# Performance work log

Measured on AMD Instinct MI355X. Metric: run time of the kernel, lower is better.

The kernel has to match this reference:

```python
import jax, jax.numpy as jnp
import numpy as np

B, S, D = 32, 256, 128
K = 16          # num_sample (negatives + the positive appended last)
V = 50000       # vocab / num_classes


def setup_inputs() -> dict:
    key = jax.random.key(0)
    k1, k2, k3, k4 = jax.random.split(key, 4)
    return {
        "input_latent": jax.random.normal(k1, (B, S, D), dtype=jnp.float32),
        "target_labels": jax.random.randint(k2, (B, S), 0, V, dtype=jnp.int64),
        "batch_samples": jax.random.randint(k3, (B, S * (K - 1)), 0, V, dtype=jnp.int64),
        "embed_weight": jax.random.normal(k4, (V, D), dtype=jnp.float32),
    }


def reference(input_latent, target_labels, batch_samples, embed_weight):
    b, s, d = input_latent.shape
    out_emb = embed_weight[target_labels]                      # [B,S,D] positives
    neg_emb = embed_weight[batch_samples].reshape(b, s, K - 1, d)
    # Candidates per target position j: K-1 negatives + the positive itself (last)
    samples = jnp.concatenate([neg_emb, out_emb[:, :, None, :]], axis=2)  # [B,S,K,D]
    # sample_rep[b,i,j,k] = latent[b,i] . samples[b,j,k]
    sample_scores = jnp.einsum('bid,bjkd->bijk', input_latent, samples)   # [B,S,S,K]
    # output_rep[b,i,j] = latent[b,i] . out_emb[b,j] (== sample_scores[...,K-1])
    out_scores = jnp.einsum('bid,bjd->bij', input_latent, out_emb)        # [B,S,S]
    # log( exp(out - max) / sum_k exp(sample - max) ) = out - logsumexp(sample)
    lse = jax.scipy.special.logsumexp(sample_scores, axis=3)              # [B,S,S]
    return out_scores - lse
```

## Files before the change

kernel.cpp:

```cpp
#include <hip/hip_runtime.h>
#include <hip/hip_bf16.h>
#include <math.h>

#define BB 32
#define SS 256
#define DD 128
#define KK 16
#define VV 50000
#define SK (SS*KK)

typedef __attribute__((ext_vector_type(8))) short bf16x8;
typedef __attribute__((ext_vector_type(4))) float f32x4;
typedef __attribute__((ext_vector_type(16))) float f32x16;
typedef unsigned short ushort_t;

static __device__ __forceinline__ short f2bf(float f) {
    __hip_bfloat16 h = __float2bfloat16(f);
    return *(short*)&h;
}

static __device__ __forceinline__ int lds_off(int row, int d) {
    return row * 256 + ((d * 2) ^ ((row & 15) << 4));
}

static __device__ __forceinline__ void gload_lds16(const void* g, void* lds) {
    __builtin_amdgcn_global_load_lds(
        (const __attribute__((address_space(1))) unsigned int*)g,
        (__attribute__((address_space(3))) unsigned int*)lds, 16, 0, 0);
}

#define NLAT (BB*SS*DD)
#define NCHUNK_LAT (NLAT/8)

__global__ __launch_bounds__(256)
void convert_lat_kernel(const float* __restrict__ latent,
                        ushort_t* __restrict__ ws_lat)
{
    int i = blockIdx.x * 256 + threadIdx.x;
    if (i >= NCHUNK_LAT) return;
    const float* src = latent + (size_t)i * 8;
    float f[8];
    *(float4*)(f + 0) = ((const float4*)src)[0];
    *(float4*)(f + 4) = ((const float4*)src)[1];
    short o[8];
    #pragma unroll
    for (int e = 0; e < 8; ++e) o[e] = f2bf(f[e]);
    *(bf16x8*)(ws_lat + (size_t)i * 8) = *(bf16x8*)o;
}

#define MTB 128
#define NT  128

__global__ __launch_bounds__(256, 5)
void neg_loss_main(const ushort_t* __restrict__ lat_bf,
                   const int*      __restrict__ labels,
                   const int*      __restrict__ samples,
                   const float*    __restrict__ embed,
                   float* __restrict__ out)
{
    __shared__ char ldsA[MTB * 256];

    const int b    = blockIdx.z;
    const int m0   = blockIdx.y * MTB;
    const int n0   = blockIdx.x * NT;
    const int tid  = threadIdx.x;
    const int wave = tid >> 6;
    const int lane = tid & 63;
    const int q    = lane & 15;
    const int sub  = lane >> 4;
    const int l31  = lane & 31;
    const int hi   = lane >> 5;

    #pragma unroll
    for (int t = 0; t < 8; ++t) {
        const int r0 = wave * 32 + t * 4;
        const int r  = r0 + sub;
        const ushort_t* src = lat_bf + ((size_t)(b * SS + m0 + r) * DD)
                                     + ((q ^ (r & 15)) << 3);
        gload_lds16(src, ldsA + r0 * 256);
    }

    const int rB  = wave * 32 + l31;
    const int gc  = n0 + rB;
    const int j   = gc >> 4;
    const int k   = gc & 15;
    const int idx = (k < 15)
        ? samples[(size_t)b * (SS * (KK - 1)) + j * (KK - 1) + k]
        : labels[b * SS + j];

    const float* rowp = embed + (size_t)idx * DD + hi * 8;
    f32x4 fb[16];
    #pragma unroll
    for (int ks = 0; ks < 8; ++ks) {
        fb[2 * ks]     = *(const f32x4*)(rowp + ks * 16);
        fb[2 * ks + 1] = *(const f32x4*)(rowp + ks * 16 + 4);
    }
    bf16x8 av[8];
    #pragma unroll
    for (int ks = 0; ks < 8; ++ks) {
        short t8[8];
        #pragma unroll
        for (int e = 0; e < 4; ++e) t8[e]     = f2bf(fb[2 * ks][e]);
        #pragma unroll
        for (int e = 0; e < 4; ++e) t8[4 + e] = f2bf(fb[2 * ks + 1][e]);
        av[ks] = *(bf16x8*)t8;
    }

    __syncthreads();

    const int jb = (n0 >> 4) + wave * 2;

    #pragma unroll
    for (int mt = 0; mt < 2; ++mt) {
        f32x16 acc0 = {}, acc1 = {};
        #pragma unroll
        for (int ks = 0; ks < 8; ++ks) {
            const int d = ks * 16 + hi * 8;
            bf16x8 bv0 = *(const bf16x8*)(ldsA + lds_off(mt * 64 + l31, d));
            bf16x8 bv1 = *(const bf16x8*)(ldsA + lds_off(mt * 64 + 32 + l31, d));
            acc0 = __builtin_amdgcn_mfma_f32_32x32x16_bf16(av[ks], bv0, acc0, 0, 0, 0);
            acc1 = __builtin_amdgcn_mfma_f32_32x32x16_bf16(av[ks], bv1, acc1, 0, 0, 0);
        }

        #pragma unroll
        for (int f = 0; f < 2; ++f) {
            const f32x16 v = f ? acc1 : acc0;
            float pm0 = fmaxf(fmaxf(fmaxf(v[0], v[1]), fmaxf(v[2], v[3])),
                              fmaxf(fmaxf(v[4], v[5]), fmaxf(v[6], v[7])));
            float pm1 = fmaxf(fmaxf(fmaxf(v[8], v[9]), fmaxf(v[10], v[11])),
                              fmaxf(fmaxf(v[12], v[13]), fmaxf(v[14], v[15])));
            float om0 = fmaxf(pm0, __shfl_xor(pm0, 32));
            float om1 = fmaxf(pm1, __shfl_xor(pm1, 32));
            float e0 = ((__expf(v[0] - om0) + __expf(v[1] - om0))
                      + (__expf(v[2] - om0) + __expf(v[3] - om0)))
                     + ((__expf(v[4] - om0) + __expf(v[5] - om0))
                      + (__expf(v[6] - om0) + __expf(v[7] - om0)));
            float e1 = ((__expf(v[8]  - om1) + __expf(v[9]  - om1))
                      + (__expf(v[10] - om1) + __expf(v[11] - om1)))
                     + ((__expf(v[12] - om1) + __expf(v[13] - om1))
                      + (__expf(v[14] - om1) + __expf(v[15] - om1)));
            float s0 = e0 + __shfl_xor(e0, 32);
            float s1 = e1 + __shfl_xor(e1, 32);
            float pos0 = __shfl_xor(v[7], 32);
            float pos1 = v[15];
            const float pos = hi ? pos1 : pos0;
            const float om  = hi ? om1  : om0;
            const float s   = hi ? s1   : s0;
            const int i = m0 + mt * 64 + f * 32 + l31;
            out[((size_t)b * SS + i) * SS + (jb + hi)] = pos - om - __logf(s);
        }
    }
}

__global__ __launch_bounds__(256)
void neg_loss_fallback(const float* __restrict__ latent,
                       const int*   __restrict__ labels,
                       const int*   __restrict__ samples,
                       const float* __restrict__ embed,
                       float* __restrict__ out)
{
    __shared__ char ldsA[64 * 256];
    __shared__ char ldsB[64 * 256];

    const int b   = blockIdx.z;
    const int m0  = blockIdx.y * 64;
    const int n0  = blockIdx.x * 64;
    const int tid = threadIdx.x;

    {
        const int r  = tid >> 2;
        const int d0 = (tid & 3) * 32;
        const float* src = latent + ((size_t)b * SS + (m0 + r)) * DD + d0;
        float f[32];
        #pragma unroll
        for (int c = 0; c < 8; ++c)
            *(float4*)(f + 4 * c) = ((const float4*)src)[c];
        #pragma unroll
        for (int c = 0; c < 4; ++c) {
            short tmp[8];
            #pragma unroll
            for (int e = 0; e < 8; ++e) tmp[e] = f2bf(f[c * 8 + e]);
            *(bf16x8*)(ldsA + lds_off(r, d0 + c * 8)) = *(bf16x8*)tmp;
        }
    }
    {
        const int c   = tid >> 2;
        const int d0  = (tid & 3) * 32;
        const int col = n0 + c;
        const int j   = col >> 4;
        const int k   = col & 15;
        const int idx = (k < 15) ? samples[(size_t)b * (SS * (KK - 1)) + j * (KK - 1) + k]
                                 : labels[b * SS + j];
        const float* src = embed + (size_t)idx * DD + d0;
        float f[32];
        #pragma unroll
        for (int cc = 0; cc < 8; ++cc)
            *(float4*)(f + 4 * cc) = ((const float4*)src)[cc];
        #pragma unroll
        for (int cc = 0; cc < 4; ++cc) {
            short tmp[8];
            #pragma unroll
            for (int e = 0; e < 8; ++e) tmp[e] = f2bf(f[cc * 8 + e]);
            *(bf16x8*)(ldsB + lds_off(c, d0 + cc * 8)) = *(bf16x8*)tmp;
        }
    }
    __syncthreads();

    const int wave = tid >> 6;
    const int lane = tid & 63;
    const int wm = wave >> 1, wn = wave & 1;
    const int lr = lane & 15;
    const int lk = (lane >> 4) * 8;
    const int sub = lane >> 4;

    f32x4 acc[2][2] = {};
    #pragma unroll
    for (int ks = 0; ks < 4; ++ks) {
        const int d = ks * 32 + lk;
        bf16x8 a[2], bb2[2];
        #pragma unroll
        for (int mf = 0; mf < 2; ++mf)
            a[mf] = *(const bf16x8*)(ldsA + lds_off(wm * 32 + mf * 16 + lr, d));
        #pragma unroll
        for (int nf = 0; nf < 2; ++nf)
            bb2[nf] = *(const bf16x8*)(ldsB + lds_off(wn * 32 + nf * 16 + lr, d));
        #pragma unroll
        for (int mf = 0; mf < 2; ++mf)
            #pragma unroll
            for (int nf = 0; nf < 2; ++nf)
                acc[mf][nf] = __builtin_amdgcn_mfma_f32_16x16x32_bf16(
                    bb2[nf], a[mf], acc[mf][nf], 0, 0, 0);
    }

    #pragma unroll
    for (int mf = 0; mf < 2; ++mf) {
        #pragma unroll
        for (int nf = 0; nf < 2; ++nf) {
            const f32x4 v = acc[mf][nf];
            float mx = fmaxf(fmaxf(v[0], v[1]), fmaxf(v[2], v[3]));
            mx = fmaxf(mx, __shfl_xor(mx, 16));
            mx = fmaxf(mx, __shfl_xor(mx, 32));
            float e = __expf(v[0] - mx) + __expf(v[1] - mx)
                    + __expf(v[2] - mx) + __expf(v[3] - mx);
            e += __shfl_xor(e, 16);
            e += __shfl_xor(e, 32);
            float pos = __shfl(v[3], (lane & 15) | 48);
            if (sub == 0) {
                const int i  = m0 + wm * 32 + mf * 16 + (lane & 15);
                const int jj = (n0 >> 4) + wn * 2 + nf;
                out[((size_t)b * SS + i) * SS + jj] = pos - mx - __logf(e);
            }
        }
    }
}

extern "C" void kernel_launch(void* const* d_in, const int* in_sizes, int n_in,
                              void* d_out, int out_size, void* d_ws, size_t ws_size,
                              hipStream_t stream) {
    const float* latent  = (const float*)d_in[0];
    const int*   labels  = (const int*)d_in[1];
    const int*   samples = (const int*)d_in[2];
    const float* embed   = (const float*)d_in[3];
    float* out = (float*)d_out;

    const size_t ws_needed = (size_t)NLAT * 2;
    if (ws_size >= ws_needed) {
        ushort_t* ws_lat = (ushort_t*)d_ws;
        convert_lat_kernel<<<(NCHUNK_LAT + 255) / 256, 256, 0, stream>>>(
            latent, ws_lat);
        dim3 grid(SK / NT, SS / MTB, BB);
        neg_loss_main<<<grid, dim3(256), 0, stream>>>(
            ws_lat, labels, samples, embed, out);
    } else {
        dim3 grid(SK / 64, SS / 64, BB);
        neg_loss_fallback<<<grid, dim3(256), 0, stream>>>(
            latent, labels, samples, embed, out);
    }
}
```

Measured before the change: 36.92 us.

## Pre-gather embedding rows to bf16 workspace and process full M per block

```diff
diff --git a/kernel.cpp b/kernel.cpp
--- a/kernel.cpp
+++ b/kernel.cpp
@@ -8,6 +8,7 @@
 #define KK 16
 #define VV 50000
 #define SK (SS*KK)
+#define NROW (BB*SK)
 
 typedef __attribute__((ext_vector_type(8))) short bf16x8;
 typedef __attribute__((ext_vector_type(4))) float f32x4;
@@ -31,37 +32,64 @@
 
 #define NLAT (BB*SS*DD)
 #define NCHUNK_LAT (NLAT/8)
+#define GB_B (NROW/64)
+#define GB_L (NCHUNK_LAT/256)
 
 __global__ __launch_bounds__(256)
-void convert_lat_kernel(const float* __restrict__ latent,
-                        ushort_t* __restrict__ ws_lat)
+void gather_kernel(const float* __restrict__ embed,
+                   const float* __restrict__ latent,
+                   const int*   __restrict__ labels,
+                   const int*   __restrict__ samples,
+                   ushort_t* __restrict__ wsB,
+                   ushort_t* __restrict__ wsLat)
 {
-    int i = blockIdx.x * 256 + threadIdx.x;
-    if (i >= NCHUNK_LAT) return;
-    const float* src = latent + (size_t)i * 8;
-    float f[8];
-    *(float4*)(f + 0) = ((const float4*)src)[0];
-    *(float4*)(f + 4) = ((const float4*)src)[1];
-    short o[8];
-    #pragma unroll
-    for (int e = 0; e < 8; ++e) o[e] = f2bf(f[e]);
-    *(bf16x8*)(ws_lat + (size_t)i * 8) = *(bf16x8*)o;
-}
-
-#define MTB 128
-#define NT  128
-
-__global__ __launch_bounds__(256, 5)
-void neg_loss_main(const ushort_t* __restrict__ lat_bf,
-                   const int*      __restrict__ labels,
-                   const int*      __restrict__ samples,
-                   const float*    __restrict__ embed,
-                   float* __restrict__ out)
+    const int gb = blockIdx.x;
+    if (gb < GB_B) {
+        const int t  = threadIdx.x;
+        const int r  = gb * 64 + (t >> 2);
+        const int qd = t & 3;
+        const int b  = r >> 12;
+        const int gc = r & 4095;
+        const int j  = gc >> 4;
+        const int k  = gc & 15;
+        const int idx = (k < 15)
+            ? samples[(size_t)b * (SS * (KK - 1)) + j * (KK - 1) + k]
+            : labels[b * SS + j];
+        const float* src = embed + (size_t)idx * DD + qd * 32;
+        float f[32];
+        #pragma unroll
+        for (int c = 0; c < 8; ++c)
+            *(f32x4*)(f + 4 * c) = *(const f32x4*)(src + 4 * c);
+        short o[32];
+        #pragma unroll
+        for (int e = 0; e < 32; ++e) o[e] = f2bf(f[e]);
+        ushort_t* dst = wsB + (size_t)r * DD + qd * 32;
+        #pragma unroll
+        for (int c = 0; c < 4; ++c)
+            *(bf16x8*)(dst + 8 * c) = *(bf16x8*)(o + 8 * c);
+    } else {
+        const int i = (gb - GB_B) * 256 + threadIdx.x;
+        const float* src = latent + (size_t)i * 8;
+        float f[8];
+        *(f32x4*)(f + 0) = ((const f32x4*)src)[0];
+        *(f32x4*)(f + 4) = ((const f32x4*)src)[1];
+        short o[8];
+        #pragma unroll
+        for (int e = 0; e < 8; ++e) o[e] = f2bf(f[e]);
+        *(bf16x8*)(wsLat + (size_t)i * 8) = *(bf16x8*)o;
+    }
+}
+
+#define NT 128
+
+__global__ __launch_bounds__(256, 2)
+void gemm_kernel(const ushort_t* __restrict__ lat_bf,
+                 const ushort_t* __restrict__ wsB,
+                 float* __restrict__ out)
 {
-    __shared__ char ldsA[MTB * 256];
-
-    const int b    = blockIdx.z;
-    const int m0   = blockIdx.y * MTB;
+    __shared__ char ldsA[SS * 256];
+
+    const int b    = blockIdx.y;
     const int n0   = blockIdx.x * NT;
     const int tid  = threadIdx.x;
     const int wave = tid >> 6;
@@ -72,46 +100,27 @@
     const int hi   = lane >> 5;
 
     #pragma unroll
-    for (int t = 0; t < 8; ++t) {
-        const int r0 = wave * 32 + t * 4;
+    for (int t = 0; t < 16; ++t) {
+        const int r0 = wave * 64 + t * 4;
         const int r  = r0 + sub;
-        const ushort_t* src = lat_bf + ((size_t)(b * SS + m0 + r) * DD)
+        const ushort_t* src = lat_bf + ((size_t)(b * SS + r) * DD)
                                      + ((q ^ (r & 15)) << 3);
         gload_lds16(src, ldsA + r0 * 256);
     }
 
-    const int rB  = wave * 32 + l31;
-    const int gc  = n0 + rB;
-    const int j   = gc >> 4;
-    const int k   = gc & 15;
-    const int idx = (k < 15)
-        ? samples[(size_t)b * (SS * (KK - 1)) + j * (KK - 1) + k]
-        : labels[b * SS + j];
-
-    const float* rowp = embed + (size_t)idx * DD + hi * 8;
-    f32x4 fb[16];
-    #pragma unroll
-    for (int ks = 0; ks < 8; ++ks) {
-        fb[2 * ks]     = *(const f32x4*)(rowp + ks * 16);
-        fb[2 * ks + 1] = *(const f32x4*)(rowp + ks * 16 + 4);
-    }
+    const int rB = wave * 32 + l31;
+    const ushort_t* rowp = wsB + ((size_t)(b * SK + n0 + rB)) * DD + hi * 8;
     bf16x8 av[8];
     #pragma unroll
-    for (int ks = 0; ks < 8; ++ks) {
-        short t8[8];
-        #pragma unroll
-        for (int e = 0; e < 4; ++e) t8[e]     = f2bf(fb[2 * ks][e]);
-        #pragma unroll
-        for (int e = 0; e < 4; ++e) t8[4 + e] = f2bf(fb[2 * ks + 1][e]);
-        av[ks] = *(bf16x8*)t8;
-    }
+    for (int ks = 0; ks < 8; ++ks)
+        av[ks] = *(const bf16x8*)(rowp + ks * 16);
 
     __syncthreads();
 
     const int jb = (n0 >> 4) + wave * 2;
 
     #pragma unroll
-    for (int mt = 0; mt < 2; ++mt) {
+    for (int mt = 0; mt < 4; ++mt) {
         f32x16 acc0 = {}, acc1 = {};
         #pragma unroll
         for (int ks = 0; ks < 8; ++ks) {
@@ -146,7 +155,7 @@
             const float pos = hi ? pos1 : pos0;
             const float om  = hi ? om1  : om0;
             const float s   = hi ? s1   : s0;
-            const int i = m0 + mt * 64 + f * 32 + l31;
+            const int i = mt * 64 + f * 32 + l31;
             out[((size_t)b * SS + i) * SS + (jb + hi)] = pos - om - __logf(s);
         }
     }
@@ -263,14 +272,14 @@
     const float* embed   = (const float*)d_in[3];
     float* out = (float*)d_out;
 
-    const size_t ws_needed = (size_t)NLAT * 2;
+    const size_t ws_needed = ((size_t)NLAT + (size_t)NROW * DD) * 2;
     if (ws_size >= ws_needed) {
-        ushort_t* ws_lat = (ushort_t*)d_ws;
-        convert_lat_kernel<<<(NCHUNK_LAT + 255) / 256, 256, 0, stream>>>(
-            latent, ws_lat);
-        dim3 grid(SK / NT, SS / MTB, BB);
-        neg_loss_main<<<grid, dim3(256), 0, stream>>>(
-            ws_lat, labels, samples, embed, out);
+        ushort_t* wsLat = (ushort_t*)d_ws;
+        ushort_t* wsB   = wsLat + NLAT;
+        gather_kernel<<<GB_B + GB_L, 256, 0, stream>>>(
+            embed, latent, labels, samples, wsB, wsLat);
+        dim3 grid(SK / NT, BB);
+        gemm_kernel<<<grid, dim3(256), 0, stream>>>(wsLat, wsB, out);
     } else {
         dim3 grid(SK / 64, SS / 64, BB);
         neg_loss_fallback<<<grid, dim3(256), 0, stream>>>(
```

New measurement: 45.08 us. 22.1% more time.

## Cover full latent row range per block and stage outputs through LDS for vector stores

Applied to the files above, without the earlier changes.

```diff
diff --git a/kernel.cpp b/kernel.cpp
--- a/kernel.cpp
+++ b/kernel.cpp
@@ -40,28 +40,27 @@
     if (i >= NCHUNK_LAT) return;
     const float* src = latent + (size_t)i * 8;
     float f[8];
-    *(float4*)(f + 0) = ((const float4*)src)[0];
-    *(float4*)(f + 4) = ((const float4*)src)[1];
+    *(f32x4*)(f + 0) = ((const f32x4*)src)[0];
+    *(f32x4*)(f + 4) = ((const f32x4*)src)[1];
     short o[8];
     #pragma unroll
     for (int e = 0; e < 8; ++e) o[e] = f2bf(f[e]);
     *(bf16x8*)(ws_lat + (size_t)i * 8) = *(bf16x8*)o;
 }
 
-#define MTB 128
-#define NT  128
-
-__global__ __launch_bounds__(256, 5)
+#define NT 128
+
+__global__ __launch_bounds__(256)
 void neg_loss_main(const ushort_t* __restrict__ lat_bf,
                    const int*      __restrict__ labels,
                    const int*      __restrict__ samples,
                    const float*    __restrict__ embed,
                    float* __restrict__ out)
 {
-    __shared__ char ldsA[MTB * 256];
-
-    const int b    = blockIdx.z;
-    const int m0   = blockIdx.y * MTB;
+    __shared__ char  ldsA[SS * 256];
+    __shared__ float trans[256][9];
+
+    const int b    = blockIdx.y;
     const int n0   = blockIdx.x * NT;
     const int tid  = threadIdx.x;
     const int wave = tid >> 6;
@@ -71,15 +70,6 @@
     const int l31  = lane & 31;
     const int hi   = lane >> 5;
 
-    #pragma unroll
-    for (int t = 0; t < 8; ++t) {
-        const int r0 = wave * 32 + t * 4;
-        const int r  = r0 + sub;
-        const ushort_t* src = lat_bf + ((size_t)(b * SS + m0 + r) * DD)
-                                     + ((q ^ (r & 15)) << 3);
-        gload_lds16(src, ldsA + r0 * 256);
-    }
-
     const int rB  = wave * 32 + l31;
     const int gc  = n0 + rB;
     const int j   = gc >> 4;
@@ -95,7 +85,19 @@
         fb[2 * ks]     = *(const f32x4*)(rowp + ks * 16);
         fb[2 * ks + 1] = *(const f32x4*)(rowp + ks * 16 + 4);
     }
-    bf16x8 av[8];
+
+    #pragma unroll
+    for (int t = 0; t < 16; ++t) {
+        const int r0 = wave * 64 + t * 4;
+        const int r  = r0 + sub;
+        const ushort_t* src = lat_bf + ((size_t)(b * SS + r) * DD)
+                                     + ((q ^ (r & 15)) << 3);
+        gload_lds16(src, ldsA + r0 * 256);
+    }
+
+    __syncthreads();
+
+    f32x16 acc[4][2] = {};
     #pragma unroll
     for (int ks = 0; ks < 8; ++ks) {
         short t8[8];
@@ -103,28 +105,23 @@
         for (int e = 0; e < 4; ++e) t8[e]     = f2bf(fb[2 * ks][e]);
         #pragma unroll
         for (int e = 0; e < 4; ++e) t8[4 + e] = f2bf(fb[2 * ks + 1][e]);
-        av[ks] = *(bf16x8*)t8;
-    }
-
-    __syncthreads();
-
-    const int jb = (n0 >> 4) + wave * 2;
-
-    #pragma unroll
-    for (int mt = 0; mt < 2; ++mt) {
-        f32x16 acc0 = {}, acc1 = {};
-        #pragma unroll
-        for (int ks = 0; ks < 8; ++ks) {
-            const int d = ks * 16 + hi * 8;
+        const bf16x8 av = *(bf16x8*)t8;
+        const int d = ks * 16 + hi * 8;
+        #pragma unroll
+        for (int mt = 0; mt < 4; ++mt) {
             bf16x8 bv0 = *(const bf16x8*)(ldsA + lds_off(mt * 64 + l31, d));
             bf16x8 bv1 = *(const bf16x8*)(ldsA + lds_off(mt * 64 + 32 + l31, d));
-            acc0 = __builtin_amdgcn_mfma_f32_32x32x16_bf16(av[ks], bv0, acc0, 0, 0, 0);
-            acc1 = __builtin_amdgcn_mfma_f32_32x32x16_bf16(av[ks], bv1, acc1, 0, 0, 0);
-        }
-
+            acc[mt][0] = __builtin_amdgcn_mfma_f32_32x32x16_bf16(av, bv0, acc[mt][0], 0, 0, 0);
+            acc[mt][1] = __builtin_amdgcn_mfma_f32_32x32x16_bf16(av, bv1, acc[mt][1], 0, 0, 0);
+        }
+    }
+
+    const int jc = wave * 2 + hi;
+    #pragma unroll
+    for (int mt = 0; mt < 4; ++mt) {
         #pragma unroll
         for (int f = 0; f < 2; ++f) {
-            const f32x16 v = f ? acc1 : acc0;
+            const f32x16 v = acc[mt][f];
             float pm0 = fmaxf(fmaxf(fmaxf(v[0], v[1]), fmaxf(v[2], v[3])),
                               fmaxf(fmaxf(v[4], v[5]), fmaxf(v[6], v[7])));
             float pm1 = fmaxf(fmaxf(fmaxf(v[8], v[9]), fmaxf(v[10], v[11])),
@@ -146,9 +143,22 @@
             const float pos = hi ? pos1 : pos0;
             const float om  = hi ? om1  : om0;
             const float s   = hi ? s1   : s0;
-            const int i = m0 + mt * 64 + f * 32 + l31;
-            out[((size_t)b * SS + i) * SS + (jb + hi)] = pos - om - __logf(s);
-        }
+            const int i = mt * 64 + f * 32 + l31;
+            trans[i][jc] = pos - om - __logf(s);
+        }
+    }
+
+    __syncthreads();
+
+    {
+        const int i  = tid;
+        const int j0 = blockIdx.x * 8;
+        float r[8];
+        #pragma unroll
+        for (int c = 0; c < 8; ++c) r[c] = trans[i][c];
+        float* dst = out + ((size_t)b * SS + i) * SS + j0;
+        *(f32x4*)(dst)     = *(f32x4*)(r);
+        *(f32x4*)(dst + 4) = *(f32x4*)(r + 4);
     }
 }
 
@@ -268,7 +278,7 @@
         ushort_t* ws_lat = (ushort_t*)d_ws;
         convert_lat_kernel<<<(NCHUNK_LAT + 255) / 256, 256, 0, stream>>>(
             latent, ws_lat);
-        dim3 grid(SK / NT, SS / MTB, BB);
+        dim3 grid(SK / NT, BB);
         neg_loss_main<<<grid, dim3(256), 0, stream>>>(
             ws_lat, labels, samples, embed, out);
     } else {
```

Measured after the change: 37.31 us. No clear change (+1.1%).
